# Kernel tuning notes

Hardware: AMD Instinct MI355X
Metric: run time of the kernel (lower is better)

## Reference

```python
import jax, jax.numpy as jnp
import numpy as np

FEATURE_DIM = 1024
B, N = 8, 2048


def setup_inputs() -> dict:
    key = jax.random.key(0)
    ks = jax.random.split(key, 7)
    s = 1.0 / np.sqrt(FEATURE_DIM)
    x = jax.random.normal(ks[0], (B, N, FEATURE_DIM), dtype=jnp.float32)
    Wk = jax.random.uniform(ks[1], (FEATURE_DIM, FEATURE_DIM), jnp.float32, -s, s)
    bk = jax.random.uniform(ks[2], (FEATURE_DIM,), jnp.float32, -s, s)
    Wq = jax.random.uniform(ks[3], (FEATURE_DIM, FEATURE_DIM), jnp.float32, -s, s)
    bq = jax.random.uniform(ks[4], (FEATURE_DIM,), jnp.float32, -s, s)
    Wv = jax.random.uniform(ks[5], (FEATURE_DIM, FEATURE_DIM), jnp.float32, -s, s)
    bv = jax.random.uniform(ks[6], (FEATURE_DIM,), jnp.float32, -s, s)
    return {"x": x, "Wq": Wq, "bq": bq, "Wk": Wk, "bk": bk, "Wv": Wv, "bv": bv}


def reference(x, Wq, bq, Wk, bk, Wv, bv):
    # Linear layers: y = x @ W.T + b (torch nn.Linear convention)
    q = jnp.einsum('bnd,ed->bne', x, Wq) + bq
    k = jnp.einsum('bnd,ed->bne', x, Wk) + bk
    v = jnp.einsum('bnd,ed->bne', x, Wv) + bv
    scale = jnp.sqrt(jnp.asarray(float(FEATURE_DIM), dtype=x.dtype))
    scores = jnp.einsum('bqd,bkd->bqk', q, k) / scale  # [B, N, N]
    weights = jax.nn.softmax(scores, axis=-1)
    attended = jnp.einsum('bqk,bkd->bqd', weights, v)
    return attended
```

## Files before the change

kernel.cpp:

```cpp
#include <hip/hip_runtime.h>
#include <cstdint>

typedef unsigned short u16;
typedef unsigned short u16x8 __attribute__((ext_vector_type(8)));
typedef __bf16 bf16x8 __attribute__((ext_vector_type(8)));
typedef float f32x4 __attribute__((ext_vector_type(4)));

#define CS2 264
#define SMEM256 131072

__device__ __forceinline__ u16 f2bf(float f) {
  uint32_t u = __float_as_uint(f);
  u += 0x7fffu + ((u >> 16) & 1u);
  return (u16)(u >> 16);
}
__device__ __forceinline__ float bf2f(u16 b) {
  return __uint_as_float(((uint32_t)b) << 16);
}

__device__ __forceinline__ void async_copy16(const void* g, void* l) {
  auto gp = reinterpret_cast<const __attribute__((address_space(1))) char*>(
      reinterpret_cast<uintptr_t>(g));
  auto lp = reinterpret_cast<__attribute__((address_space(3))) char*>(
      static_cast<uint32_t>(reinterpret_cast<uintptr_t>(l)));
  __builtin_amdgcn_global_load_lds(gp, lp, 16, 0, 0);
}

__device__ __forceinline__ void barrier_() {
  asm volatile("" ::: "memory");
  __builtin_amdgcn_s_barrier();
  asm volatile("" ::: "memory");
}
#define VMC(N) asm volatile("s_waitcnt vmcnt(" #N ")" ::: "memory")

template <int NT, int LDA, int LDB>
__device__ __forceinline__ void gemm256(const u16* __restrict__ gA,
                                        const u16* __restrict__ gB, char* lds,
                                        f32x4 (&acc)[8][4]) {
  const int t = threadIdx.x;
  const int w = t >> 6, l = t & 63;
  const int lm = l & 15, lq = l >> 4;
  const int wr = w & 1, wc = w >> 1;

  const u16* gAt = gA + (long)(t >> 3) * LDA + ((t & 7) ^ ((t >> 3) & 7)) * 8;
  const u16* gBt = gB + (long)(t >> 3) * LDB + ((t & 7) ^ ((t >> 3) & 7)) * 8;
  char* ldsw = lds + w * 1024;

  bf16x8 a[8], b0[4], b1[4];

  auto stA = [&](int P, int h, int kt) {
#pragma unroll
    for (int s = 0; s < 2; s++)
      async_copy16(gAt + (long)(h * 128 + s * 64) * LDA + kt * 64,
                   ldsw + P * 65536 + h * 16384 + s * 8192);
  };
  auto stB = [&](int P, int h, int kt) {
#pragma unroll
    for (int s = 0; s < 2; s++)
      async_copy16(gBt + (long)(h * 128 + s * 64) * LDB + kt * 64,
                   ldsw + P * 65536 + 32768 + h * 16384 + s * 8192);
  };
  auto rdA = [&](int P, int h) {
#pragma unroll
    for (int il = 0; il < 4; il++) {
      const int r = wr * 64 + il * 16 + lm;
      const char* base = lds + P * 65536 + h * 16384 + r * 128;
#pragma unroll
      for (int ks = 0; ks < 2; ks++)
        a[il * 2 + ks] = *(const bf16x8*)(base + ((ks * 4 + lq) ^ (r & 7)) * 16);
    }
  };
  auto rdB = [&](bf16x8(&b)[4], int P, int h) {
#pragma unroll
    for (int jl = 0; jl < 2; jl++) {
      const int r = wc * 32 + jl * 16 + lm;
      const char* base = lds + P * 65536 + 32768 + h * 16384 + r * 128;
#pragma unroll
      for (int ks = 0; ks < 2; ks++)
        b[jl * 2 + ks] = *(const bf16x8*)(base + ((ks * 4 + lq) ^ (r & 7)) * 16);
    }
  };
  auto mma = [&](int mh, int nh, const bf16x8(&b)[4]) {
    __builtin_amdgcn_s_setprio(1);
#pragma unroll
    for (int ks = 0; ks < 2; ks++)
#pragma unroll
      for (int il = 0; il < 4; il++)
#pragma unroll
        for (int jl = 0; jl < 2; jl++)
          acc[mh * 4 + il][nh * 2 + jl] =
              __builtin_amdgcn_mfma_f32_16x16x32_bf16(
                  a[il * 2 + ks], b[jl * 2 + ks], acc[mh * 4 + il][nh * 2 + jl],
                  0, 0, 0);
    __builtin_amdgcn_s_setprio(0);
  };

  stA(0, 0, 0); stB(0, 0, 0); stB(0, 1, 0); stA(0, 1, 0);
  stA(1, 0, 1); stB(1, 0, 1); stB(1, 1, 1);
  VMC(6);
  barrier_();

#pragma unroll 1
  for (int i = 0; i < NT / 2 - 1; ++i) {
    const int kt = 2 * i;
    rdA(0, 0); rdB(b0, 0, 0);
    stA(1, 1, kt + 1);
    barrier_(); mma(0, 0, b0); barrier_();
    rdB(b1, 0, 1);
    stA(0, 0, kt + 2);
    barrier_(); mma(0, 1, b1); barrier_();
    rdA(0, 1);
    stB(0, 0, kt + 2);
    barrier_(); mma(1, 0, b0); barrier_();
    stB(0, 1, kt + 2);
    barrier_(); mma(1, 1, b1);
    VMC(6);
    barrier_();
    rdA(1, 0); rdB(b0, 1, 0);
    stA(0, 1, kt + 2);
    barrier_(); mma(0, 0, b0); barrier_();
    rdB(b1, 1, 1);
    stA(1, 0, kt + 3);
    barrier_(); mma(0, 1, b1); barrier_();
    rdA(1, 1);
    stB(1, 0, kt + 3);
    barrier_(); mma(1, 0, b0); barrier_();
    stB(1, 1, kt + 3);
    barrier_(); mma(1, 1, b1);
    VMC(6);
    barrier_();
  }
  rdA(0, 0); rdB(b0, 0, 0);
  stA(1, 1, NT - 1);
  barrier_(); mma(0, 0, b0); barrier_();
  rdB(b1, 0, 1);
  barrier_(); mma(0, 1, b1); barrier_();
  rdA(0, 1);
  barrier_(); mma(1, 0, b0); barrier_();
  barrier_(); mma(1, 1, b1);
  VMC(0);
  barrier_();
  rdA(1, 0); rdB(b0, 1, 0);
  barrier_(); mma(0, 0, b0); barrier_();
  rdB(b1, 1, 1);
  barrier_(); mma(0, 1, b1); barrier_();
  rdA(1, 1);
  barrier_(); mma(1, 0, b0); barrier_();
  mma(1, 1, b1);
  barrier_();
}

__device__ __forceinline__ void epi256_bf16(char* lds, f32x4 (&acc)[8][4],
                                            u16* __restrict__ Cp, int ldc,
                                            const float* __restrict__ bias) {
  const int t = threadIdx.x, w = t >> 6, l = t & 63;
  const int lm = l & 15, lq = l >> 4;
  const int wr = w & 1, wc = w >> 1;
  u16* Cs = (u16*)lds;
#pragma unroll
  for (int mh = 0; mh < 2; mh++) {
#pragma unroll
    for (int j = 0; j < 4; j++) {
      const int ncol = (j >> 1) * 128 + wc * 32 + (j & 1) * 16 + lm;
      const float bj = bias ? bias[ncol] : 0.f;
#pragma unroll
      for (int il = 0; il < 4; il++) {
        const int rrow = wr * 64 + il * 16 + lq * 4;
#pragma unroll
        for (int r = 0; r < 4; r++)
          Cs[(rrow + r) * CS2 + ncol] = f2bf(acc[mh * 4 + il][j][r] + bj);
      }
    }
    __syncthreads();
#pragma unroll
    for (int it = 0; it < 8; it++) {
      const int row = it * 16 + (t >> 5);
      u16x8 v = *(const u16x8*)(Cs + row * CS2 + (t & 31) * 8);
      *(u16x8*)(Cp + (long)(mh * 128 + row) * ldc + (t & 31) * 8) = v;
    }
    __syncthreads();
  }
}

__device__ __forceinline__ void convert_chunk(const float* x, const float* Wq,
                                              const float* Wk, const float* Wv,
                                              u16* xb, u16* Wb, int c) {
  const float* src;
  u16* dst;
  int off;
  if (c < 4194304) {
    src = x; dst = xb; off = c;
  } else {
    int j = c - 4194304;
    int sel = j >> 18;
    off = j & 262143;
    src = (sel == 0) ? Wq : (sel == 1) ? Wk : Wv;
    dst = Wb + (long)sel * 1048576;
  }
  float4 f = ((const float4*)src)[off];
  ((ushort4*)dst)[off] = make_ushort4(f2bf(f.x), f2bf(f.y), f2bf(f.z),
                                      f2bf(f.w));
}

__global__ __launch_bounds__(256) void k_convert(const float* x,
                                                 const float* Wq,
                                                 const float* Wk,
                                                 const float* Wv, u16* xb,
                                                 u16* Wb, float* rs) {
  const int c = blockIdx.x * 256 + threadIdx.x;
  if (c < 4980736) {
    convert_chunk(x, Wq, Wk, Wv, xb, Wb, c);
  } else if (rs) {
    ((float4*)rs)[c - 4980736] = make_float4(0.f, 0.f, 0.f, 0.f);
  }
}

__global__ __launch_bounds__(512, 2) void k_qkv256(
    const u16* xb, const u16* Wb, u16* qb, u16* kb, u16* vt,
    const float* bq, const float* bk, const float* bv) {
  __shared__ __align__(16) char lds[SMEM256];
  const int bid = blockIdx.x;
  const int xcd = bid & 7, lid = bid >> 3;
  const int by = xcd * 8 + (lid & 7);
  const int bx = lid >> 3;
  f32x4 acc[8][4] = {};
  gemm256<16, 1024, 1024>(xb + (long)by * 256 * 1024,
                          Wb + (long)bx * 256 * 1024, lds, acc);
  const int t = threadIdx.x, w = t >> 6, l = t & 63;
  const int lm = l & 15, lq = l >> 4;
  const int wr = w & 1, wc = w >> 1;
  const int sec = bx >> 2;
  const int nl = (bx & 3) * 256;
  const float* bias = (sec == 0) ? bq : (sec == 1) ? bk : bv;
  u16* Cs = (u16*)lds;
  if (sec < 2) {
    u16* Cp = ((sec == 0) ? qb : kb) + (long)by * 256 * 1024 + nl;
    epi256_bf16(lds, acc, Cp, 1024, bias + nl);
  } else {
    const int m0 = by * 256, b = m0 >> 11, ml = m0 & 2047;
#pragma unroll
    for (int nh = 0; nh < 2; nh++) {
#pragma unroll
      for (int jl = 0; jl < 2; jl++) {
        const int j = nh * 2 + jl;
        const int nloc = wc * 32 + jl * 16 + lm;
        const float bj = bias[nl + nh * 128 + nloc];
#pragma unroll
        for (int i = 0; i < 8; i++) {
          const int mloc = (i >> 2) * 128 + wr * 64 + (i & 3) * 16 + lq * 4;
          *(ushort4*)(Cs + nloc * CS2 + mloc) =
              make_ushort4(f2bf(acc[i][j][0] + bj), f2bf(acc[i][j][1] + bj),
                           f2bf(acc[i][j][2] + bj), f2bf(acc[i][j][3] + bj));
        }
      }
      __syncthreads();
      u16* Vp = vt + ((long)b * 1024 + nl + nh * 128) * 2048 + ml;
#pragma unroll
      for (int it = 0; it < 8; it++) {
        const int nrow = it * 16 + (t >> 5);
        u16x8 v = *(const u16x8*)(Cs + nrow * CS2 + (t & 31) * 8);
        *(u16x8*)(Vp + (long)nrow * 2048 + (t & 31) * 8) = v;
      }
      __syncthreads();
    }
  }
}

__global__ __launch_bounds__(512, 2) void k_s256(const u16* qb, const u16* kb,
                                                 u16* S, float* rowsum) {
  __shared__ __align__(16) char lds[SMEM256];
  const int bid = blockIdx.x;
  const int xcd = bid & 7, lid = bid >> 3;
  const int z = lid >> 3, s = lid & 7;
  const int m = (xcd & 1) * 4 + (s & 3);
  const int n = (xcd >> 1) * 2 + (s >> 2);
  f32x4 acc[8][4] = {};
  gemm256<16, 1024, 1024>(qb + (long)z * 2048 * 1024 + (long)m * 256 * 1024,
                          kb + (long)z * 2048 * 1024 + (long)n * 256 * 1024,
                          lds, acc);
  const int t = threadIdx.x, w = t >> 6, l = t & 63;
  const int lm = l & 15, lq = l >> 4;
  const int wr = w & 1;
#pragma unroll
  for (int i = 0; i < 8; i++)
#pragma unroll
    for (int j = 0; j < 4; j++)
#pragma unroll
      for (int r = 0; r < 4; r++)
        acc[i][j][r] = __expf(acc[i][j][r] * 0.03125f);
  if (rowsum) {
#pragma unroll
    for (int i = 0; i < 8; i++)
#pragma unroll
      for (int r = 0; r < 4; r++) {
        float p = acc[i][0][r] + acc[i][1][r] + acc[i][2][r] + acc[i][3][r];
        p += __shfl_xor(p, 1);
        p += __shfl_xor(p, 2);
        p += __shfl_xor(p, 4);
        p += __shfl_xor(p, 8);
        if (lm == 0)
          atomicAdd(&rowsum[z * 2048 + m * 256 + (i >> 2) * 128 + wr * 64 +
                            (i & 3) * 16 + lq * 4 + r],
                    p);
      }
  }
  epi256_bf16(lds, acc,
              S + (long)z * 2048 * 2048 + (long)m * 256 * 2048 + n * 256, 2048,
              nullptr);
}

__global__ __launch_bounds__(256) void k_rowsum(const u16* S, float* rowsum) {
  __shared__ float red[4];
  const long row = blockIdx.x;
  const int t = threadIdx.x, w = t >> 6, l = t & 63;
  uint4 raw = ((const uint4*)(S + row * 2048))[t];
  float s = bf2f((u16)(raw.x & 0xffff)) + bf2f((u16)(raw.x >> 16)) +
            bf2f((u16)(raw.y & 0xffff)) + bf2f((u16)(raw.y >> 16)) +
            bf2f((u16)(raw.z & 0xffff)) + bf2f((u16)(raw.z >> 16)) +
            bf2f((u16)(raw.w & 0xffff)) + bf2f((u16)(raw.w >> 16));
#pragma unroll
  for (int o = 32; o; o >>= 1) s += __shfl_xor(s, o);
  if (l == 0) red[w] = s;
  __syncthreads();
  if (t == 0) rowsum[row] = red[0] + red[1] + red[2] + red[3];
}

__global__ __launch_bounds__(512, 2) void k_pv256(const u16* S, const u16* vt,
                                                  const float* rowsum,
                                                  u16* Obf, float* outf,
                                                  int direct_out) {
  __shared__ __align__(16) char lds[SMEM256];
  const int bid = blockIdx.x;
  const int xcd = bid & 7, lid = bid >> 3;
  const int z = lid >> 2, s = lid & 3;
  const int m = (xcd & 3) * 2 + (s & 1);
  const int n = (xcd >> 2) * 2 + (s >> 1);
  f32x4 acc[8][4] = {};
  gemm256<32, 2048, 2048>(S + (long)z * 2048 * 2048 + (long)m * 256 * 2048,
                          vt + (long)z * 1024 * 2048 + (long)n * 256 * 2048,
                          lds, acc);
  const int t = threadIdx.x, w = t >> 6, l = t & 63;
  const int lm = l & 15, lq = l >> 4;
  const int wr = w & 1, wc = w >> 1;
#pragma unroll
  for (int i = 0; i < 8; i++)
#pragma unroll
    for (int r = 0; r < 4; r++) {
      const float inv = 1.0f / rowsum[z * 2048 + m * 256 + (i >> 2) * 128 +
                                      wr * 64 + (i & 3) * 16 + lq * 4 + r];
#pragma unroll
      for (int j = 0; j < 4; j++) acc[i][j][r] *= inv;
    }
  if (direct_out) {
    float* Cf = outf + (long)z * 2048 * 1024 + (long)m * 256 * 1024 + n * 256;
#pragma unroll
    for (int i = 0; i < 8; i++) {
      const int gm = (i >> 2) * 128 + wr * 64 + (i & 3) * 16 + lq * 4;
#pragma unroll
      for (int j = 0; j < 4; j++) {
        const int gn = (j >> 1) * 128 + wc * 32 + (j & 1) * 16 + lm;
#pragma unroll
        for (int r = 0; r < 4; r++)
          Cf[(long)(gm + r) * 1024 + gn] = acc[i][j][r];
      }
    }
  } else {
    epi256_bf16(lds, acc,
                Obf + (long)z * 2048 * 1024 + (long)m * 256 * 1024 + n * 256,
                1024, nullptr);
  }
}

__global__ __launch_bounds__(256) void k_expand(const u16* in, float* out) {
  int i = blockIdx.x * 256 + threadIdx.x;
  if (i >= 4194304) return;
  ushort4 u = ((const ushort4*)in)[i];
  ((float4*)out)[i] = make_float4(bf2f(u.x), bf2f(u.y), bf2f(u.z), bf2f(u.w));
}

extern "C" void kernel_launch(void* const* d_in, const int* in_sizes, int n_in,
                              void* d_out, int out_size, void* d_ws,
                              size_t ws_size, hipStream_t stream) {
  const float* x = (const float*)d_in[0];
  const float* Wq = (const float*)d_in[1];
  const float* bq = (const float*)d_in[2];
  const float* Wk = (const float*)d_in[3];
  const float* bk = (const float*)d_in[4];
  const float* Wv = (const float*)d_in[5];
  const float* bv = (const float*)d_in[6];

  const long MN = 16384L * 1024;
  u16* slot0 = (u16*)d_ws;
  u16* slot1 = slot0 + MN;
  u16* slot2 = slot1 + MN;
  u16* slot3 = slot2 + MN;
  u16* xb = (u16*)d_out;
  u16* Wb = xb + MN;

  const int bigws =
      ws_size >= (size_t)(5 * MN) * sizeof(u16) + 65536 ? 1 : 0;
  u16* S = bigws ? slot3 : (u16*)d_out;
  float* rowsum = bigws ? (float*)(slot3 + 8L * 2048 * 2048)
                        : (float*)slot0;
  u16* Obf = slot0 + 32768;
  float* outf = (float*)d_out;

  dim3 blk(256), blk5(512);
  k_convert<<<dim3(19472), blk, 0, stream>>>(x, Wq, Wk, Wv, xb, Wb,
                                             bigws ? rowsum : nullptr);
  k_qkv256<<<dim3(768), blk5, 0, stream>>>(xb, Wb, slot0, slot1, slot2, bq,
                                           bk, bv);
  if (bigws) {
    k_s256<<<dim3(512), blk5, 0, stream>>>(slot0, slot1, S, rowsum);
    k_pv256<<<dim3(256), blk5, 0, stream>>>(S, slot2, rowsum, nullptr, outf,
                                            1);
  } else {
    k_s256<<<dim3(512), blk5, 0, stream>>>(slot0, slot1, S, nullptr);
    k_rowsum<<<dim3(16384), blk, 0, stream>>>(S, rowsum);
    k_pv256<<<dim3(256), blk5, 0, stream>>>(S, slot2, rowsum, Obf, nullptr,
                                            0);
    k_expand<<<dim3(16384), blk, 0, stream>>>(Obf, outf);
  }
}
```

Baseline: 364.3 us.

## Double-buffer A/B register fragments to overlap LDS reads with MFMA in GEMM

Adds a second set of A and B register fragments so LDS reads for the next sub-tile are issued before the MFMAs of the current sub-tile, rotating buffers across the four quadrants and across iterations. The global-to-LDS async copy schedule and the vmcnt waits are reshuffled to fit. The aim is to hide LDS read latency behind matrix math. In exchange it uses more VGPRs, which may reduce occupancy, and the reordered waits carry a risk of subtle hazards.

```diff
diff --git a/kernel.cpp b/kernel.cpp
--- a/kernel.cpp
+++ b/kernel.cpp
@@ -46,7 +46,7 @@
   const u16* gBt = gB + (long)(t >> 3) * LDB + ((t & 7) ^ ((t >> 3) & 7)) * 8;
   char* ldsw = lds + w * 1024;
 
-  bf16x8 a[8], b0[4], b1[4];
+  bf16x8 aA[8], aB[8], bA[4], bB[4];
 
   auto stA = [&](int P, int h, int kt) {
 #pragma unroll
@@ -60,7 +60,7 @@
       async_copy16(gBt + (long)(h * 128 + s * 64) * LDB + kt * 64,
                    ldsw + P * 65536 + 32768 + h * 16384 + s * 8192);
   };
-  auto rdA = [&](int P, int h) {
+  auto rdA = [&](bf16x8(&a)[8], int P, int h) {
 #pragma unroll
     for (int il = 0; il < 4; il++) {
       const int r = wr * 64 + il * 16 + lm;
@@ -80,7 +80,7 @@
         b[jl * 2 + ks] = *(const bf16x8*)(base + ((ks * 4 + lq) ^ (r & 7)) * 16);
     }
   };
-  auto mma = [&](int mh, int nh, const bf16x8(&b)[4]) {
+  auto mma = [&](int mh, int nh, const bf16x8(&a)[8], const bf16x8(&b)[4]) {
     __builtin_amdgcn_s_setprio(1);
 #pragma unroll
     for (int ks = 0; ks < 2; ks++)
@@ -99,54 +99,47 @@
   stA(1, 0, 1); stB(1, 0, 1); stB(1, 1, 1);
   VMC(6);
   barrier_();
+  rdA(aA, 0, 0); rdB(bA, 0, 0);
 
 #pragma unroll 1
   for (int i = 0; i < NT / 2 - 1; ++i) {
     const int kt = 2 * i;
-    rdA(0, 0); rdB(b0, 0, 0);
-    stA(1, 1, kt + 1);
-    barrier_(); mma(0, 0, b0); barrier_();
-    rdB(b1, 0, 1);
-    stA(0, 0, kt + 2);
-    barrier_(); mma(0, 1, b1); barrier_();
-    rdA(0, 1);
+    stA(1, 1, kt + 1); rdB(bB, 0, 1);
+    barrier_(); mma(0, 0, aA, bA); barrier_();
+    stA(0, 0, kt + 2); rdA(aB, 0, 1);
+    barrier_(); mma(0, 1, aA, bB); barrier_();
     stB(0, 0, kt + 2);
-    barrier_(); mma(1, 0, b0); barrier_();
-    stB(0, 1, kt + 2);
-    barrier_(); mma(1, 1, b1);
-    VMC(6);
+    barrier_(); mma(1, 0, aB, bA);
+    VMC(4);
     barrier_();
-    rdA(1, 0); rdB(b0, 1, 0);
-    stA(0, 1, kt + 2);
-    barrier_(); mma(0, 0, b0); barrier_();
-    rdB(b1, 1, 1);
-    stA(1, 0, kt + 3);
-    barrier_(); mma(0, 1, b1); barrier_();
-    rdA(1, 1);
+    stB(0, 1, kt + 2); rdA(aA, 1, 0); rdB(bA, 1, 0);
+    barrier_(); mma(1, 1, aB, bB); barrier_();
+    stA(0, 1, kt + 2); rdB(bB, 1, 1);
+    barrier_(); mma(0, 0, aA, bA); barrier_();
+    stA(1, 0, kt + 3); rdA(aB, 1, 1);
+    barrier_(); mma(0, 1, aA, bB); barrier_();
     stB(1, 0, kt + 3);
-    barrier_(); mma(1, 0, b0); barrier_();
-    stB(1, 1, kt + 3);
-    barrier_(); mma(1, 1, b1);
-    VMC(6);
+    barrier_(); mma(1, 0, aB, bA);
+    VMC(4);
     barrier_();
-  }
-  rdA(0, 0); rdB(b0, 0, 0);
-  stA(1, 1, NT - 1);
-  barrier_(); mma(0, 0, b0); barrier_();
-  rdB(b1, 0, 1);
-  barrier_(); mma(0, 1, b1); barrier_();
-  rdA(0, 1);
-  barrier_(); mma(1, 0, b0); barrier_();
-  barrier_(); mma(1, 1, b1);
+    stB(1, 1, kt + 3); rdA(aA, 0, 0); rdB(bA, 0, 0);
+    barrier_(); mma(1, 1, aB, bB); barrier_();
+  }
+  stA(1, 1, NT - 1); rdB(bB, 0, 1);
+  barrier_(); mma(0, 0, aA, bA); barrier_();
+  rdA(aB, 0, 1);
+  barrier_(); mma(0, 1, aA, bB); barrier_();
+  barrier_(); mma(1, 0, aB, bA);
   VMC(0);
   barrier_();
-  rdA(1, 0); rdB(b0, 1, 0);
-  barrier_(); mma(0, 0, b0); barrier_();
-  rdB(b1, 1, 1);
-  barrier_(); mma(0, 1, b1); barrier_();
-  rdA(1, 1);
-  barrier_(); mma(1, 0, b0); barrier_();
-  mma(1, 1, b1);
+  rdA(aA, 1, 0); rdB(bA, 1, 0);
+  barrier_(); mma(1, 1, aB, bB); barrier_();
+  rdB(bB, 1, 1);
+  barrier_(); mma(0, 0, aA, bA); barrier_();
+  rdA(aB, 1, 1);
+  barrier_(); mma(0, 1, aA, bB); barrier_();
+  barrier_(); mma(1, 0, aB, bA); barrier_();
+  mma(1, 1, aB, bB);
   barrier_();
 }
 
```

New measurement: 716.2 us. 1.97x slower.

## Reschedule GEMM main loop to overlap LDS reads with MFMA and halve barriers

Applied to the files above, without the earlier changes.

Restructures the software pipeline of the 256-tile GEMM mainloop. LDS fragment reads for the next sub-step now follow each MFMA group directly, and the extra barrier after each mma is gone, so each phase uses one barrier. The prologue preloads one less B half and does the first fragment reads before the loop, with waitcnt thresholds adjusted to match. This aims to cut synchronization stalls and hide LDS latency behind MFMA, but it risks LDS read/write hazards if the buffer reuse order is wrong.

```diff
diff --git a/kernel.cpp b/kernel.cpp
--- a/kernel.cpp
+++ b/kernel.cpp
@@ -96,57 +96,44 @@
   };
 
   stA(0, 0, 0); stB(0, 0, 0); stB(0, 1, 0); stA(0, 1, 0);
-  stA(1, 0, 1); stB(1, 0, 1); stB(1, 1, 1);
-  VMC(6);
+  stA(1, 0, 1); stB(1, 0, 1);
+  VMC(4);
   barrier_();
+  rdA(0, 0); rdB(b0, 0, 0);
 
 #pragma unroll 1
   for (int i = 0; i < NT / 2 - 1; ++i) {
     const int kt = 2 * i;
-    rdA(0, 0); rdB(b0, 0, 0);
+    stB(1, 1, kt + 1);
+    barrier_(); mma(0, 0, b0); rdB(b1, 0, 1);
     stA(1, 1, kt + 1);
-    barrier_(); mma(0, 0, b0); barrier_();
-    rdB(b1, 0, 1);
+    barrier_(); mma(0, 1, b1); rdA(0, 1);
     stA(0, 0, kt + 2);
-    barrier_(); mma(0, 1, b1); barrier_();
-    rdA(0, 1);
+    barrier_(); mma(1, 0, b0);
     stB(0, 0, kt + 2);
-    barrier_(); mma(1, 0, b0); barrier_();
+    VMC(4);
+    barrier_(); mma(1, 1, b1); rdA(1, 0); rdB(b0, 1, 0);
     stB(0, 1, kt + 2);
-    barrier_(); mma(1, 1, b1);
-    VMC(6);
-    barrier_();
-    rdA(1, 0); rdB(b0, 1, 0);
+    barrier_(); mma(0, 0, b0); rdB(b1, 1, 1);
     stA(0, 1, kt + 2);
-    barrier_(); mma(0, 0, b0); barrier_();
-    rdB(b1, 1, 1);
+    barrier_(); mma(0, 1, b1); rdA(1, 1);
     stA(1, 0, kt + 3);
-    barrier_(); mma(0, 1, b1); barrier_();
-    rdA(1, 1);
+    barrier_(); mma(1, 0, b0);
     stB(1, 0, kt + 3);
-    barrier_(); mma(1, 0, b0); barrier_();
-    stB(1, 1, kt + 3);
-    barrier_(); mma(1, 1, b1);
-    VMC(6);
-    barrier_();
-  }
-  rdA(0, 0); rdB(b0, 0, 0);
+    VMC(4);
+    barrier_(); mma(1, 1, b1); rdA(0, 0); rdB(b0, 0, 0);
+  }
+  stB(1, 1, NT - 1);
+  barrier_(); mma(0, 0, b0); rdB(b1, 0, 1);
   stA(1, 1, NT - 1);
-  barrier_(); mma(0, 0, b0); barrier_();
-  rdB(b1, 0, 1);
-  barrier_(); mma(0, 1, b1); barrier_();
-  rdA(0, 1);
-  barrier_(); mma(1, 0, b0); barrier_();
+  barrier_(); mma(0, 1, b1); rdA(0, 1);
+  barrier_(); mma(1, 0, b0);
+  VMC(0);
+  barrier_(); mma(1, 1, b1); rdA(1, 0); rdB(b0, 1, 0);
+  barrier_(); mma(0, 0, b0); rdB(b1, 1, 1);
+  barrier_(); mma(0, 1, b1); rdA(1, 1);
+  barrier_(); mma(1, 0, b0);
   barrier_(); mma(1, 1, b1);
-  VMC(0);
-  barrier_();
-  rdA(1, 0); rdB(b0, 1, 0);
-  barrier_(); mma(0, 0, b0); barrier_();
-  rdB(b1, 1, 1);
-  barrier_(); mma(0, 1, b1); barrier_();
-  rdA(1, 1);
-  barrier_(); mma(1, 0, b0); barrier_();
-  mma(1, 1, b1);
   barrier_();
 }
 
```

Result: no change. 358.8 us (-1.5%).
